# Optimization experiments

Hardware: AMD Instinct MI355X
Metric: run time of the kernel (lower is better)

## Reference

```python
import jax, jax.numpy as jnp
import numpy as np

N = 100000      # num_nodes
E = 1200000     # num_edges (avg degree 12)
F_IN = 64       # num_features
H = 64          # args.hidden_dim
C = 40          # num_classes


def setup_inputs() -> dict:
    key = jax.random.key(0)
    ks = jax.random.split(key, 8)
    x = jax.random.normal(ks[0], (N, F_IN), jnp.float32)
    edge_index = jax.random.randint(ks[1], (2, E), 0, N, dtype=jnp.int64)
    edge_attr = jax.random.uniform(ks[2], (E,), jnp.float32)

    def glorot(k, fi, fo):
        return jax.random.normal(k, (fi, fo), jnp.float32) * jnp.sqrt(2.0 / (fi + fo))

    return {
        "x": x, "edge_index": edge_index, "edge_attr": edge_attr,
        "W1": glorot(ks[3], F_IN, H), "b1": jnp.zeros((H,), jnp.float32),
        "W2": glorot(ks[4], H, H),    "b2": jnp.zeros((H,), jnp.float32),
        "W3": glorot(ks[5], H, H),    "b3": jnp.zeros((H,), jnp.float32),
        "W4": glorot(ks[6], H, C),    "b4": jnp.zeros((C,), jnp.float32),
    }


def _gcn_layer(h, W, b, src, dst, norm):
    # GCNConv: linear transform, gather source features, weight by symmetric
    # norm, scatter-add at targets, add bias.
    h = h @ W                                   # [N, out]
    msg = h[src] * norm[:, None]                # [E+N, out]
    out = jax.ops.segment_sum(msg, dst, num_segments=N)
    return out + b


def reference(x, edge_index, edge_attr, W1, b1, W2, b2, W3, b3, W4, b4):
    # Add self-loops with weight 1 (PyG GCNConv default fill_value=1.)
    loop = jnp.arange(N, dtype=edge_index.dtype)
    src = jnp.concatenate([edge_index[0], loop])
    dst = jnp.concatenate([edge_index[1], loop])
    w = jnp.concatenate([edge_attr, jnp.ones((N,), edge_attr.dtype)])
    # Symmetric normalization: deg^{-1/2}[src] * w * deg^{-1/2}[dst]
    deg = jax.ops.segment_sum(w, dst, num_segments=N)
    dis = jnp.where(deg > 0, jax.lax.rsqrt(jnp.maximum(deg, 1e-12)), 0.0)
    norm = dis[src] * w * dis[dst]

    h = jax.nn.elu(_gcn_layer(x, W1, b1, src, dst, norm))
    h = jax.nn.elu(_gcn_layer(h, W2, b2, src, dst, norm))
    h = jax.nn.elu(_gcn_layer(h, W3, b3, src, dst, norm))
    h = _gcn_layer(h, W4, b4, src, dst, norm)
    return jax.nn.log_softmax(h, axis=1)
```

## Files before the change

### kernel.cpp

```cpp
#include <hip/hip_runtime.h>
#include <hip/hip_fp16.h>
#include <cstdint>
#include <cmath>


#define NPB_SHIFT 9
#define NPB 512
#define CHUNK 4096

__device__ __forceinline__ float fdot2f(__half2 a, __half2 b, float c) {
#if defined(__has_builtin)
#if __has_builtin(__builtin_amdgcn_fdot2)
    typedef _Float16 h2v __attribute__((ext_vector_type(2)));
    return __builtin_amdgcn_fdot2(__builtin_bit_cast(h2v, a),
                                  __builtin_bit_cast(h2v, b), c, false);
#else
    float2 fa = __half22float2(a), fb = __half22float2(b);
    return fmaf(fa.x, fb.x, fmaf(fa.y, fb.y, c));
#endif
#else
    float2 fa = __half22float2(a), fb = __half22float2(b);
    return fmaf(fa.x, fb.x, fmaf(fa.y, fb.y, c));
#endif
}


__global__ __launch_bounds__(256) void bucket_init_kernel(int* __restrict__ bucket_cnt,
                                                          int nbuck) {
    if ((int)threadIdx.x < nbuck) bucket_cnt[threadIdx.x] = 0;
}

__global__ __launch_bounds__(256) void bucket_count_kernel(const int* __restrict__ dst,
                                                           int* __restrict__ bucket_cnt,
                                                           int* __restrict__ blockbase,
                                                           int nbuck, int E) {
    __shared__ int hist[256];
    int tid = threadIdx.x;
    hist[tid] = 0;
    __syncthreads();
    int base = blockIdx.x * CHUNK;
    #pragma unroll
    for (int u = 0; u < CHUNK / 256; ++u) {
        int e = base + u * 256 + tid;
        if (e < E) atomicAdd(&hist[dst[e] >> NPB_SHIFT], 1);
    }
    __syncthreads();
    if (tid < nbuck)
        blockbase[blockIdx.x * nbuck + tid] = atomicAdd(&bucket_cnt[tid], hist[tid]);
}

__global__ __launch_bounds__(64) void bucket_scan_kernel(const int* __restrict__ bucket_cnt,
                                                         int* __restrict__ bucket_base,
                                                         int nbuck, int E) {
    int lane = threadIdx.x;
    int run = 0;
    for (int b0 = 0; b0 < nbuck; b0 += 64) {
        int i = b0 + lane;
        int v = (i < nbuck) ? bucket_cnt[i] : 0;
        int x = v;
        #pragma unroll
        for (int off = 1; off < 64; off <<= 1) {
            int t = __shfl_up(x, off);
            if (lane >= off) x += t;
        }
        if (i < nbuck) bucket_base[i] = run + x - v;
        run += __shfl(x, 63);
    }
    if (lane == 0) bucket_base[nbuck] = E;
}

__global__ __launch_bounds__(256) void bucket_scatter_kernel(const int* __restrict__ src,
                                                             const int* __restrict__ dst,
                                                             const float* __restrict__ w,
                                                             const int* __restrict__ bucket_base,
                                                             const int* __restrict__ blockbase,
                                                             int2* __restrict__ temp,
                                                             int nbuck, int E) {
    __shared__ int cursor[256];
    int tid = threadIdx.x;
    if (tid < nbuck)
        cursor[tid] = bucket_base[tid] + blockbase[blockIdx.x * nbuck + tid];
    __syncthreads();
    int base = blockIdx.x * CHUNK;
    #pragma unroll
    for (int u = 0; u < CHUNK / 256; ++u) {
        int e = base + u * 256 + tid;
        if (e < E) {
            int d = dst[e];
            int pos = atomicAdd(&cursor[d >> NPB_SHIFT], 1);
            temp[pos] = make_int2(src[e] | ((d & (NPB - 1)) << 17),
                                  __float_as_int(w[e]));
        }
    }
}

__global__ __launch_bounds__(256) void bucket_csr_kernel(const int2* __restrict__ temp,
                                                         const int* __restrict__ bucket_base,
                                                         int* __restrict__ offsets,
                                                         int2* __restrict__ pairs,
                                                         int n, int E) {
    __shared__ int cnt[NPB];
    __shared__ int wtot[4];
    int tid = threadIdx.x;
    int bk = blockIdx.x;
    int base = bucket_base[bk], end = bucket_base[bk + 1];
    cnt[tid] = 0; cnt[tid + 256] = 0;
    __syncthreads();
    for (int j = base + tid; j < end; j += 256)
        atomicAdd(&cnt[temp[j].x >> 17], 1);
    __syncthreads();
    int a0 = cnt[2 * tid], a1 = cnt[2 * tid + 1];
    int s = a0 + a1;
    int lane = tid & 63, wid = tid >> 6;
    int x = s;
    #pragma unroll
    for (int off = 1; off < 64; off <<= 1) {
        int t2 = __shfl_up(x, off);
        if (lane >= off) x += t2;
    }
    if (lane == 63) wtot[wid] = x;
    __syncthreads();
    int wbase = 0;
    #pragma unroll
    for (int wv = 0; wv < 4; ++wv) if (wv < wid) wbase += wtot[wv];
    int e0 = wbase + x - s;
    int abs0 = base + e0, abs1 = base + e0 + a0;
    int node0 = bk * NPB + 2 * tid;
    if (node0 < n)     offsets[node0]     = abs0;
    if (node0 + 1 < n) offsets[node0 + 1] = abs1;
    __syncthreads();
    cnt[2 * tid] = abs0; cnt[2 * tid + 1] = abs1;
    __syncthreads();
    for (int j = base + tid; j < end; j += 256) {
        int2 t2 = temp[j];
        int pos = atomicAdd(&cnt[t2.x >> 17], 1);
        pairs[pos] = make_int2(t2.x & 0x1FFFF, t2.y);
    }
    if (bk == 0 && tid == 0) offsets[n] = E;
}

__global__ __launch_bounds__(256) void rowsum_scale_kernel(const int* __restrict__ offsets,
                                                           const int2* __restrict__ pairs,
                                                           const float* __restrict__ x,
                                                           float* __restrict__ dis,
                                                           __half* __restrict__ g, int n) {
    int node = blockIdx.x * 16 + (threadIdx.x >> 4);
    int q = threadIdx.x & 15;
    if (node >= n) return;
    int j0 = offsets[node], end = offsets[node + 1];
    float s = 0.f;
    for (int j = j0 + q; j < end; j += 16) s += __int_as_float(pairs[j].y);
    #pragma unroll
    for (int off = 8; off; off >>= 1) s += __shfl_xor(s, off);
    float dn = rsqrtf(1.0f + s);
    if (q == 0) dis[node] = dn;
    float4 v = reinterpret_cast<const float4*>(x)[(size_t)node * 16 + q];
    __half2 pk[2];
    pk[0] = __float22half2_rn(make_float2(dn * v.x, dn * v.y));
    pk[1] = __float22half2_rn(make_float2(dn * v.z, dn * v.w));
    reinterpret_cast<float2*>(g + (size_t)node * 64)[q] = *reinterpret_cast<float2*>(pk);
}

__device__ __forceinline__ void accum8(float* acc, float4 rv, float w) {
    const __half2* h = reinterpret_cast<const __half2*>(&rv);
    #pragma unroll
    for (int k = 0; k < 4; ++k) {
        float2 f = __half22float2(h[k]);
        acc[2 * k]     = fmaf(w, f.x, acc[2 * k]);
        acc[2 * k + 1] = fmaf(w, f.y, acc[2 * k + 1]);
    }
}

__device__ __forceinline__ void agg_node(const float4* __restrict__ gt,
                                         const int2* __restrict__ pairs,
                                         int j, int end, int node, int q,
                                         float* __restrict__ acc) {
    for (; j + 4 <= end; j += 4) {
        int2 p0 = pairs[j], p1 = pairs[j + 1], p2 = pairs[j + 2], p3 = pairs[j + 3];
        float4 r0 = gt[(size_t)p0.x * 8 + q];
        float4 r1 = gt[(size_t)p1.x * 8 + q];
        float4 r2 = gt[(size_t)p2.x * 8 + q];
        float4 r3 = gt[(size_t)p3.x * 8 + q];
        accum8(acc, r0, __int_as_float(p0.y));
        accum8(acc, r1, __int_as_float(p1.y));
        accum8(acc, r2, __int_as_float(p2.y));
        accum8(acc, r3, __int_as_float(p3.y));
    }
    for (; j < end; ++j) {
        int2 p = pairs[j];
        float4 r = gt[(size_t)p.x * 8 + q];
        accum8(acc, r, __int_as_float(p.y));
    }
    float4 rs = gt[(size_t)node * 8 + q];
    accum8(acc, rs, 1.0f);
}

__global__ __launch_bounds__(256) void layer_fused_kernel(const __half* __restrict__ gin,
                                                          const float* __restrict__ dis,
                                                          const int* __restrict__ offsets,
                                                          const int2* __restrict__ pairs,
                                                          const float* __restrict__ W,
                                                          const float* __restrict__ b,
                                                          __half* __restrict__ gout, int n) {
    __shared__ __half2 rows[32][33];
    __shared__ __half2 WT[64][32];
    __shared__ float bias_s[64];
    for (int idx = threadIdx.x; idx < 64 * 32; idx += 256) {
        int k2 = idx >> 6, c = idx & 63;
        WT[c][k2] = __float22half2_rn(make_float2(W[(2 * k2) * 64 + c],
                                                  W[(2 * k2 + 1) * 64 + c]));
    }
    if (threadIdx.x < 64) bias_s[threadIdx.x] = b[threadIdx.x];

    int tid = threadIdx.x;
    {
        int ln = tid >> 3;
        int q  = tid & 7;
        int gnode = blockIdx.x * 32 + ln;
        if (gnode < n) {
            const float4* gt = reinterpret_cast<const float4*>(gin);
            float acc[8] = {0.f, 0.f, 0.f, 0.f, 0.f, 0.f, 0.f, 0.f};
            agg_node(gt, pairs, offsets[gnode], offsets[gnode + 1], gnode, q, acc);
            float dn = dis[gnode];
            #pragma unroll
            for (int k2 = 0; k2 < 4; ++k2)
                rows[ln][q * 4 + k2] =
                    __float22half2_rn(make_float2(dn * acc[2 * k2], dn * acc[2 * k2 + 1]));
        }
    }
    __syncthreads();
    {
        int node2  = tid & 31;
        int slice  = tid >> 5;
        int gnode2 = blockIdx.x * 32 + node2;
        if (gnode2 < n) {
            __half2 h2[32];
            #pragma unroll
            for (int i = 0; i < 32; ++i) h2[i] = rows[node2][i];

            float dn = dis[gnode2];
            int c0 = slice * 8;
            float r[8];
            #pragma unroll
            for (int cc = 0; cc < 8; ++cc) {
                const __half2* wt = &WT[c0 + cc][0];
                float a0 = 0.f, a1 = 0.f, a2 = 0.f, a3 = 0.f;
                #pragma unroll
                for (int i = 0; i < 8; ++i) {
                    a0 = fdot2f(h2[4 * i],     wt[4 * i],     a0);
                    a1 = fdot2f(h2[4 * i + 1], wt[4 * i + 1], a1);
                    a2 = fdot2f(h2[4 * i + 2], wt[4 * i + 2], a2);
                    a3 = fdot2f(h2[4 * i + 3], wt[4 * i + 3], a3);
                }
                float v = (a0 + a1) + (a2 + a3) + bias_s[c0 + cc];
                v = (v > 0.f) ? v : expm1f(v);
                r[cc] = dn * v;
            }
            __half2 pk[4];
            pk[0] = __float22half2_rn(make_float2(r[0], r[1]));
            pk[1] = __float22half2_rn(make_float2(r[2], r[3]));
            pk[2] = __float22half2_rn(make_float2(r[4], r[5]));
            pk[3] = __float22half2_rn(make_float2(r[6], r[7]));
            *reinterpret_cast<float4*>(gout + (size_t)gnode2 * 64 + c0) =
                *reinterpret_cast<float4*>(pk);
        }
    }
}

__global__ __launch_bounds__(256) void aggregate_kernel(const __half* __restrict__ g,
                                                        const float* __restrict__ dis,
                                                        const int* __restrict__ offsets,
                                                        const int2* __restrict__ pairs,
                                                        __half* __restrict__ aggout, int n) {
    int node = blockIdx.x * 32 + (threadIdx.x >> 3);
    int q = threadIdx.x & 7;
    if (node >= n) return;
    const float4* gt = reinterpret_cast<const float4*>(g);
    float acc[8] = {0.f, 0.f, 0.f, 0.f, 0.f, 0.f, 0.f, 0.f};
    agg_node(gt, pairs, offsets[node], offsets[node + 1], node, q, acc);
    float dn = dis[node];
    __half2 o[4];
    o[0] = __float22half2_rn(make_float2(dn * acc[0], dn * acc[1]));
    o[1] = __float22half2_rn(make_float2(dn * acc[2], dn * acc[3]));
    o[2] = __float22half2_rn(make_float2(dn * acc[4], dn * acc[5]));
    o[3] = __float22half2_rn(make_float2(dn * acc[6], dn * acc[7]));
    reinterpret_cast<float4*>(aggout)[(size_t)node * 8 + q] = *reinterpret_cast<float4*>(o);
}

__global__ __launch_bounds__(256) void gemm40_softmax_kernel(const __half* __restrict__ in,
                                                             const float* __restrict__ W,
                                                             const float* __restrict__ b,
                                                             float* __restrict__ out, int n) {
    __shared__ __half2 WT[40][32];
    for (int idx = threadIdx.x; idx < 40 * 32; idx += 256) {
        int c = idx % 40, k2 = idx / 40;
        WT[c][k2] = __float22half2_rn(make_float2(W[(2 * k2) * 40 + c],
                                                  W[(2 * k2 + 1) * 40 + c]));
    }
    __syncthreads();

    int row = blockIdx.x * 256 + threadIdx.x;
    if (row >= n) return;

    __half2 h2[32];
    const float4* inp = reinterpret_cast<const float4*>(in + (size_t)row * 64);
    #pragma unroll
    for (int i = 0; i < 8; ++i) {
        float4 raw = inp[i];
        const __half2* hp = reinterpret_cast<const __half2*>(&raw);
        h2[4 * i] = hp[0]; h2[4 * i + 1] = hp[1];
        h2[4 * i + 2] = hp[2]; h2[4 * i + 3] = hp[3];
    }

    float r[40];
    #pragma unroll 2
    for (int c = 0; c < 40; ++c) {
        const __half2* wt = &WT[c][0];
        float a0 = 0.f, a1 = 0.f, a2 = 0.f, a3 = 0.f;
        #pragma unroll
        for (int i = 0; i < 8; ++i) {
            a0 = fdot2f(h2[4 * i],     wt[4 * i],     a0);
            a1 = fdot2f(h2[4 * i + 1], wt[4 * i + 1], a1);
            a2 = fdot2f(h2[4 * i + 2], wt[4 * i + 2], a2);
            a3 = fdot2f(h2[4 * i + 3], wt[4 * i + 3], a3);
        }
        r[c] = (a0 + a1) + (a2 + a3) + b[c];
    }

    float m = r[0];
    #pragma unroll
    for (int c = 1; c < 40; ++c) m = fmaxf(m, r[c]);
    float s = 0.f;
    #pragma unroll
    for (int c = 0; c < 40; ++c) s += expf(r[c] - m);
    float ls = logf(s) + m;

    float* outp = out + (size_t)row * 40;
    #pragma unroll
    for (int c4 = 0; c4 < 10; ++c4) {
        *reinterpret_cast<float4*>(outp + c4 * 4) =
            make_float4(r[c4 * 4] - ls, r[c4 * 4 + 1] - ls,
                        r[c4 * 4 + 2] - ls, r[c4 * 4 + 3] - ls);
    }
}


static inline size_t align_up(size_t x, size_t a) { return (x + a - 1) & ~(a - 1); }

extern "C" void kernel_launch(void* const* d_in, const int* in_sizes, int n_in,
                              void* d_out, int out_size, void* d_ws, size_t ws_size,
                              hipStream_t stream) {
    const float* x  = (const float*)d_in[0];
    const int*   ei = (const int*)d_in[1];
    const float* ea = (const float*)d_in[2];
    const float* W1 = (const float*)d_in[3];
    const float* b1 = (const float*)d_in[4];
    const float* W2 = (const float*)d_in[5];
    const float* b2 = (const float*)d_in[6];
    const float* W3 = (const float*)d_in[7];
    const float* b3 = (const float*)d_in[8];
    const float* W4 = (const float*)d_in[9];
    const float* b4 = (const float*)d_in[10];

    const int N = in_sizes[0] / 64;
    const int E = in_sizes[1] / 2;

    const int* src = ei;
    const int* dst = ei + E;

    const int nbuck   = (N + NPB - 1) >> NPB_SHIFT;
    const int nblk_ac = (E + CHUNK - 1) / CHUNK;

    char* p = (char*)d_ws;
    int*    offsets     = (int*)p;  p += align_up(((size_t)N + 1) * 4, 256);
    int*    bucket_cnt  = (int*)p;  p += align_up(((size_t)nbuck + 1) * 4, 256);
    int*    bucket_base = (int*)p;  p += align_up(((size_t)nbuck + 1) * 4, 256);
    int*    blockbase   = (int*)p;  p += align_up((size_t)nblk_ac * nbuck * 4, 256);
    float*  dis         = (float*)p; p += align_up((size_t)N * 4, 256);
    int2*   pairs       = (int2*)p;  p += align_up(((size_t)E + 8) * 8, 256);
    int2*   temp        = (int2*)p;  p += align_up(((size_t)E + 8) * 8, 256);
    __half* gA          = (__half*)p; p += align_up((size_t)N * 64 * 2, 256);
    __half* gB          = (__half*)p; p += align_up((size_t)N * 64 * 2, 256);
    (void)ws_size;

    const int nb_n   = (N + 255) / 256;
    const int nb_g16 = (N + 15) / 16;
    const int nb_f   = (N + 31) / 32;

    bucket_init_kernel<<<1, 256, 0, stream>>>(bucket_cnt, nbuck);
    bucket_count_kernel<<<nblk_ac, 256, 0, stream>>>(dst, bucket_cnt, blockbase, nbuck, E);
    bucket_scan_kernel<<<1, 64, 0, stream>>>(bucket_cnt, bucket_base, nbuck, E);
    bucket_scatter_kernel<<<nblk_ac, 256, 0, stream>>>(src, dst, ea, bucket_base,
                                                       blockbase, temp, nbuck, E);
    bucket_csr_kernel<<<nbuck, 256, 0, stream>>>(temp, bucket_base, offsets, pairs, N, E);
    rowsum_scale_kernel<<<nb_g16, 256, 0, stream>>>(offsets, pairs, x, dis, gA, N);

    layer_fused_kernel<<<nb_f, 256, 0, stream>>>(gA, dis, offsets, pairs, W1, b1, gB, N);
    layer_fused_kernel<<<nb_f, 256, 0, stream>>>(gB, dis, offsets, pairs, W2, b2, gA, N);
    layer_fused_kernel<<<nb_f, 256, 0, stream>>>(gA, dis, offsets, pairs, W3, b3, gB, N);

    aggregate_kernel<<<nb_f, 256, 0, stream>>>(gB, dis, offsets, pairs, gA, N);
    gemm40_softmax_kernel<<<nb_n, 256, 0, stream>>>(gA, W4, b4, (float*)d_out, N);
}
```

Measured before the change: 222.8 us.

## Fuse final aggregation with GEMM40 and log-softmax; use wave-local LDS sync

Merges the last aggregate kernel and the separate 40-class GEMM plus log-softmax into one kernel. Each wave aggregates 8 nodes into LDS, and the same wave then does the dense transform and a shuffle-based log-softmax. This removes one launch and the round trip of the intermediate half buffer. The block-wide barrier between the aggregate and transform phases is replaced by a wave-level LDS fence, with the thread-to-node mapping reorganised so each wave only reads rows it wrote. WT rows are padded to avoid bank conflicts. The output is now written as scalar stores of 5 floats per thread instead of float4 rows.

```diff
diff --git a/kernel.cpp b/kernel.cpp
--- a/kernel.cpp
+++ b/kernel.cpp
@@ -24,6 +24,12 @@
 #endif
 }
 
+__device__ __forceinline__ void wave_lds_fence() {
+    asm volatile("s_waitcnt lgkmcnt(0)" ::: "memory");
+    __builtin_amdgcn_wave_barrier();
+    __builtin_amdgcn_sched_barrier(0);
+}
+
 
 __global__ __launch_bounds__(256) void bucket_init_kernel(int* __restrict__ bucket_cnt,
                                                           int nbuck) {
@@ -195,6 +201,27 @@
     accum8(acc, rs, 1.0f);
 }
 
+__device__ __forceinline__ void phase1_agg(const __half* __restrict__ gin,
+                                           const float* __restrict__ dis,
+                                           const int* __restrict__ offsets,
+                                           const int2* __restrict__ pairs,
+                                           __half2 (*rows)[33], int n, int tid,
+                                           int blockbase_node) {
+    int ln = tid >> 3;
+    int q  = tid & 7;
+    int gnode = blockbase_node + ln;
+    if (gnode < n) {
+        const float4* gt = reinterpret_cast<const float4*>(gin);
+        float acc[8] = {0.f, 0.f, 0.f, 0.f, 0.f, 0.f, 0.f, 0.f};
+        agg_node(gt, pairs, offsets[gnode], offsets[gnode + 1], gnode, q, acc);
+        float dn = dis[gnode];
+        #pragma unroll
+        for (int k2 = 0; k2 < 4; ++k2)
+            rows[ln][q * 4 + k2] =
+                __float22half2_rn(make_float2(dn * acc[2 * k2], dn * acc[2 * k2 + 1]));
+    }
+}
+
 __global__ __launch_bounds__(256) void layer_fused_kernel(const __half* __restrict__ gin,
                                                           const float* __restrict__ dis,
                                                           const int* __restrict__ offsets,
@@ -203,7 +230,7 @@
                                                           const float* __restrict__ b,
                                                           __half* __restrict__ gout, int n) {
     __shared__ __half2 rows[32][33];
-    __shared__ __half2 WT[64][32];
+    __shared__ __half2 WT[64][33];
     __shared__ float bias_s[64];
     for (int idx = threadIdx.x; idx < 64 * 32; idx += 256) {
         int k2 = idx >> 6, c = idx & 63;
@@ -211,136 +238,113 @@
                                                   W[(2 * k2 + 1) * 64 + c]));
     }
     if (threadIdx.x < 64) bias_s[threadIdx.x] = b[threadIdx.x];
+    __syncthreads();
 
     int tid = threadIdx.x;
-    {
-        int ln = tid >> 3;
-        int q  = tid & 7;
-        int gnode = blockIdx.x * 32 + ln;
-        if (gnode < n) {
-            const float4* gt = reinterpret_cast<const float4*>(gin);
-            float acc[8] = {0.f, 0.f, 0.f, 0.f, 0.f, 0.f, 0.f, 0.f};
-            agg_node(gt, pairs, offsets[gnode], offsets[gnode + 1], gnode, q, acc);
-            float dn = dis[gnode];
+    phase1_agg(gin, dis, offsets, pairs, rows, n, tid, blockIdx.x * 32);
+    wave_lds_fence();
+
+    int lane  = tid & 63, wave = tid >> 6;
+    int node2 = wave * 8 + (lane & 7);
+    int slice = lane >> 3;
+    int gnode2 = blockIdx.x * 32 + node2;
+    if (gnode2 < n) {
+        __half2 h2[32];
+        #pragma unroll
+        for (int i = 0; i < 32; ++i) h2[i] = rows[node2][i];
+        float dn = dis[gnode2];
+        int c0 = slice * 8;
+        float r[8];
+        #pragma unroll
+        for (int cc = 0; cc < 8; ++cc) {
+            const __half2* wt = &WT[c0 + cc][0];
+            float a0 = 0.f, a1 = 0.f, a2 = 0.f, a3 = 0.f;
             #pragma unroll
-            for (int k2 = 0; k2 < 4; ++k2)
-                rows[ln][q * 4 + k2] =
-                    __float22half2_rn(make_float2(dn * acc[2 * k2], dn * acc[2 * k2 + 1]));
+            for (int i = 0; i < 8; ++i) {
+                a0 = fdot2f(h2[4 * i],     wt[4 * i],     a0);
+                a1 = fdot2f(h2[4 * i + 1], wt[4 * i + 1], a1);
+                a2 = fdot2f(h2[4 * i + 2], wt[4 * i + 2], a2);
+                a3 = fdot2f(h2[4 * i + 3], wt[4 * i + 3], a3);
+            }
+            float v = (a0 + a1) + (a2 + a3) + bias_s[c0 + cc];
+            v = (v > 0.f) ? v : expm1f(v);
+            r[cc] = dn * v;
         }
-    }
-    __syncthreads();
-    {
-        int node2  = tid & 31;
-        int slice  = tid >> 5;
-        int gnode2 = blockIdx.x * 32 + node2;
-        if (gnode2 < n) {
-            __half2 h2[32];
-            #pragma unroll
-            for (int i = 0; i < 32; ++i) h2[i] = rows[node2][i];
-
-            float dn = dis[gnode2];
-            int c0 = slice * 8;
-            float r[8];
-            #pragma unroll
-            for (int cc = 0; cc < 8; ++cc) {
-                const __half2* wt = &WT[c0 + cc][0];
-                float a0 = 0.f, a1 = 0.f, a2 = 0.f, a3 = 0.f;
-                #pragma unroll
-                for (int i = 0; i < 8; ++i) {
-                    a0 = fdot2f(h2[4 * i],     wt[4 * i],     a0);
-                    a1 = fdot2f(h2[4 * i + 1], wt[4 * i + 1], a1);
-                    a2 = fdot2f(h2[4 * i + 2], wt[4 * i + 2], a2);
-                    a3 = fdot2f(h2[4 * i + 3], wt[4 * i + 3], a3);
-                }
-                float v = (a0 + a1) + (a2 + a3) + bias_s[c0 + cc];
-                v = (v > 0.f) ? v : expm1f(v);
-                r[cc] = dn * v;
-            }
-            __half2 pk[4];
-            pk[0] = __float22half2_rn(make_float2(r[0], r[1]));
-            pk[1] = __float22half2_rn(make_float2(r[2], r[3]));
-            pk[2] = __float22half2_rn(make_float2(r[4], r[5]));
-            pk[3] = __float22half2_rn(make_float2(r[6], r[7]));
-            *reinterpret_cast<float4*>(gout + (size_t)gnode2 * 64 + c0) =
-                *reinterpret_cast<float4*>(pk);
-        }
-    }
-}
-
-__global__ __launch_bounds__(256) void aggregate_kernel(const __half* __restrict__ g,
-                                                        const float* __restrict__ dis,
-                                                        const int* __restrict__ offsets,
-                                                        const int2* __restrict__ pairs,
-                                                        __half* __restrict__ aggout, int n) {
-    int node = blockIdx.x * 32 + (threadIdx.x >> 3);
-    int q = threadIdx.x & 7;
-    if (node >= n) return;
-    const float4* gt = reinterpret_cast<const float4*>(g);
-    float acc[8] = {0.f, 0.f, 0.f, 0.f, 0.f, 0.f, 0.f, 0.f};
-    agg_node(gt, pairs, offsets[node], offsets[node + 1], node, q, acc);
-    float dn = dis[node];
-    __half2 o[4];
-    o[0] = __float22half2_rn(make_float2(dn * acc[0], dn * acc[1]));
-    o[1] = __float22half2_rn(make_float2(dn * acc[2], dn * acc[3]));
-    o[2] = __float22half2_rn(make_float2(dn * acc[4], dn * acc[5]));
-    o[3] = __float22half2_rn(make_float2(dn * acc[6], dn * acc[7]));
-    reinterpret_cast<float4*>(aggout)[(size_t)node * 8 + q] = *reinterpret_cast<float4*>(o);
-}
-
-__global__ __launch_bounds__(256) void gemm40_softmax_kernel(const __half* __restrict__ in,
-                                                             const float* __restrict__ W,
-                                                             const float* __restrict__ b,
-                                                             float* __restrict__ out, int n) {
-    __shared__ __half2 WT[40][32];
+        __half2 pk[4];
+        pk[0] = __float22half2_rn(make_float2(r[0], r[1]));
+        pk[1] = __float22half2_rn(make_float2(r[2], r[3]));
+        pk[2] = __float22half2_rn(make_float2(r[4], r[5]));
+        pk[3] = __float22half2_rn(make_float2(r[6], r[7]));
+        *reinterpret_cast<float4*>(gout + (size_t)gnode2 * 64 + c0) =
+            *reinterpret_cast<float4*>(pk);
+    }
+}
+
+__global__ __launch_bounds__(256) void layer4_fused_kernel(const __half* __restrict__ gin,
+                                                           const float* __restrict__ dis,
+                                                           const int* __restrict__ offsets,
+                                                           const int2* __restrict__ pairs,
+                                                           const float* __restrict__ W,
+                                                           const float* __restrict__ b,
+                                                           float* __restrict__ out, int n) {
+    __shared__ __half2 rows[32][33];
+    __shared__ __half2 WT[40][33];
+    __shared__ float bias_s[40];
     for (int idx = threadIdx.x; idx < 40 * 32; idx += 256) {
         int c = idx % 40, k2 = idx / 40;
         WT[c][k2] = __float22half2_rn(make_float2(W[(2 * k2) * 40 + c],
                                                   W[(2 * k2 + 1) * 40 + c]));
     }
-    __syncthreads();
-
-    int row = blockIdx.x * 256 + threadIdx.x;
-    if (row >= n) return;
-
-    __half2 h2[32];
-    const float4* inp = reinterpret_cast<const float4*>(in + (size_t)row * 64);
-    #pragma unroll
-    for (int i = 0; i < 8; ++i) {
-        float4 raw = inp[i];
-        const __half2* hp = reinterpret_cast<const __half2*>(&raw);
-        h2[4 * i] = hp[0]; h2[4 * i + 1] = hp[1];
-        h2[4 * i + 2] = hp[2]; h2[4 * i + 3] = hp[3];
-    }
-
-    float r[40];
-    #pragma unroll 2
-    for (int c = 0; c < 40; ++c) {
-        const __half2* wt = &WT[c][0];
-        float a0 = 0.f, a1 = 0.f, a2 = 0.f, a3 = 0.f;
-        #pragma unroll
-        for (int i = 0; i < 8; ++i) {
-            a0 = fdot2f(h2[4 * i],     wt[4 * i],     a0);
-            a1 = fdot2f(h2[4 * i + 1], wt[4 * i + 1], a1);
-            a2 = fdot2f(h2[4 * i + 2], wt[4 * i + 2], a2);
-            a3 = fdot2f(h2[4 * i + 3], wt[4 * i + 3], a3);
+    if (threadIdx.x < 40) bias_s[threadIdx.x] = b[threadIdx.x];
+    __syncthreads();
+
+    int tid = threadIdx.x;
+    phase1_agg(gin, dis, offsets, pairs, rows, n, tid, blockIdx.x * 32);
+    wave_lds_fence();
+
+    int lane  = tid & 63, wave = tid >> 6;
+    int node2 = wave * 8 + (lane & 7);
+    int slice = lane >> 3;
+    int gnode2 = blockIdx.x * 32 + node2;
+
+    float r[5];
+    float mp = -__builtin_inff();
+    if (gnode2 < n) {
+        __half2 h2[32];
+        #pragma unroll
+        for (int i = 0; i < 32; ++i) h2[i] = rows[node2][i];
+        int c0 = slice * 5;
+        #pragma unroll
+        for (int cc = 0; cc < 5; ++cc) {
+            const __half2* wt = &WT[c0 + cc][0];
+            float a0 = 0.f, a1 = 0.f, a2 = 0.f, a3 = 0.f;
+            #pragma unroll
+            for (int i = 0; i < 8; ++i) {
+                a0 = fdot2f(h2[4 * i],     wt[4 * i],     a0);
+                a1 = fdot2f(h2[4 * i + 1], wt[4 * i + 1], a1);
+                a2 = fdot2f(h2[4 * i + 2], wt[4 * i + 2], a2);
+                a3 = fdot2f(h2[4 * i + 3], wt[4 * i + 3], a3);
+            }
+            r[cc] = (a0 + a1) + (a2 + a3) + bias_s[c0 + cc];
+            mp = fmaxf(mp, r[cc]);
         }
-        r[c] = (a0 + a1) + (a2 + a3) + b[c];
-    }
-
-    float m = r[0];
-    #pragma unroll
-    for (int c = 1; c < 40; ++c) m = fmaxf(m, r[c]);
-    float s = 0.f;
-    #pragma unroll
-    for (int c = 0; c < 40; ++c) s += expf(r[c] - m);
-    float ls = logf(s) + m;
-
-    float* outp = out + (size_t)row * 40;
-    #pragma unroll
-    for (int c4 = 0; c4 < 10; ++c4) {
-        *reinterpret_cast<float4*>(outp + c4 * 4) =
-            make_float4(r[c4 * 4] - ls, r[c4 * 4 + 1] - ls,
-                        r[c4 * 4 + 2] - ls, r[c4 * 4 + 3] - ls);
+    }
+    mp = fmaxf(mp, __shfl_xor(mp, 8));
+    mp = fmaxf(mp, __shfl_xor(mp, 16));
+    mp = fmaxf(mp, __shfl_xor(mp, 32));
+    float sp = 0.f;
+    if (gnode2 < n) {
+        #pragma unroll
+        for (int cc = 0; cc < 5; ++cc) sp += expf(r[cc] - mp);
+    }
+    sp += __shfl_xor(sp, 8);
+    sp += __shfl_xor(sp, 16);
+    sp += __shfl_xor(sp, 32);
+    if (gnode2 < n) {
+        float ls = logf(sp) + mp;
+        float* outp = out + (size_t)gnode2 * 40 + slice * 5;
+        #pragma unroll
+        for (int cc = 0; cc < 5; ++cc) outp[cc] = r[cc] - ls;
     }
 }
 
@@ -383,7 +387,6 @@
     __half* gB          = (__half*)p; p += align_up((size_t)N * 64 * 2, 256);
     (void)ws_size;
 
-    const int nb_n   = (N + 255) / 256;
     const int nb_g16 = (N + 15) / 16;
     const int nb_f   = (N + 31) / 32;
 
@@ -399,6 +402,6 @@
     layer_fused_kernel<<<nb_f, 256, 0, stream>>>(gB, dis, offsets, pairs, W2, b2, gA, N);
     layer_fused_kernel<<<nb_f, 256, 0, stream>>>(gA, dis, offsets, pairs, W3, b3, gB, N);
 
-    aggregate_kernel<<<nb_f, 256, 0, stream>>>(gB, dis, offsets, pairs, gA, N);
-    gemm40_softmax_kernel<<<nb_n, 256, 0, stream>>>(gA, W4, b4, (float*)d_out, N);
-}
+    layer4_fused_kernel<<<nb_f, 256, 0, stream>>>(gB, dis, offsets, pairs, W4, b4,
+                                                  (float*)d_out, N);
+}
```

Result: faster. 207.7 us (-6.8%).
